# Kernel optimization log

Measured on AMD Instinct MI355X. Metric: run time of the kernel, lower is better.

The kernel has to match this reference:

```python
import jax, jax.numpy as jnp
import numpy as np

EMBED_DIM = 1024
NUM_HEADS = 16
HEAD_DIM = EMBED_DIM // NUM_HEADS
B, S = 4, 2048


def setup_inputs() -> dict:
    key = jax.random.key(0)
    ks = jax.random.split(key, 11)
    sc = 1.0 / np.sqrt(EMBED_DIM)
    return {
        "query": jax.random.normal(ks[0], (B, S, EMBED_DIM), jnp.float32),
        "key": jax.random.normal(ks[1], (B, S, EMBED_DIM), jnp.float32),
        "value": jax.random.normal(ks[2], (B, S, EMBED_DIM), jnp.float32),
        "Wq": jax.random.normal(ks[3], (EMBED_DIM, EMBED_DIM), jnp.float32) * sc,
        "Wk": jax.random.normal(ks[4], (EMBED_DIM, EMBED_DIM), jnp.float32) * sc,
        "Wv": jax.random.normal(ks[5], (EMBED_DIM, EMBED_DIM), jnp.float32) * sc,
        "Wo": jax.random.normal(ks[6], (EMBED_DIM, EMBED_DIM), jnp.float32) * sc,
        "bq": jax.random.normal(ks[7], (EMBED_DIM,), jnp.float32) * 0.01,
        "bk": jax.random.normal(ks[8], (EMBED_DIM,), jnp.float32) * 0.01,
        "bv": jax.random.normal(ks[9], (EMBED_DIM,), jnp.float32) * 0.01,
        "bo": jax.random.normal(ks[10], (EMBED_DIM,), jnp.float32) * 0.01,
    }


def reference(query, key, value, Wq, Wk, Wv, Wo, bq, bk, bv, bo):
    # QKV projections: [B,S,E] @ [E,E] (torch Linear uses x @ W.T; here W stored pre-transposed)
    def split_heads(x):  # [B,S,E] -> [B,H,S,D]
        Bx, Sx, _ = x.shape
        return x.reshape(Bx, Sx, NUM_HEADS, HEAD_DIM).transpose(0, 2, 1, 3)

    Q = split_heads(query @ Wq + bq)
    K = split_heads(key @ Wk + bk)
    V = split_heads(value @ Wv + bv)

    scale = 1.0 / np.sqrt(HEAD_DIM).astype(np.float32)
    scores = jnp.einsum("bhqd,bhkd->bhqk", Q, K) * scale  # [B,H,Sq,Sk]
    attn = jax.nn.softmax(scores, axis=-1)
    ctx = jnp.einsum("bhqk,bhkd->bhqd", attn, V)  # [B,H,Sq,D]
    ctx = ctx.transpose(0, 2, 1, 3).reshape(query.shape[0], query.shape[1], EMBED_DIM)
    return ctx @ Wo + bo
```

## Files before the change

kernel.cpp:

```cpp
#include <hip/hip_runtime.h>
#include <hip/hip_bf16.h>

typedef unsigned short u16;
typedef unsigned int u32;
typedef __attribute__((ext_vector_type(8))) short bf16x8;
typedef __attribute__((ext_vector_type(4))) float f32x4;
typedef __attribute__((ext_vector_type(2))) unsigned u32x2v;

constexpr int Bn = 4;
constexpr int Sn = 2048;
constexpr int En = 1024;
constexpr int Hn = 16;
constexpr int Dn = 64;
constexpr int Kd = 1024;

__device__ __forceinline__ u16 f2b(float f) {
  union { float f; unsigned u; } v; v.f = f;
  unsigned u = v.u;
  return (u16)((u + 0x7fffu + ((u >> 16) & 1u)) >> 16);
}

__device__ __forceinline__ u32 cvtpk_bf16(float lo, float hi) {
  u32 r;
  asm("v_cvt_pk_bf16_f32 %0, %1, %2" : "=v"(r) : "v"(lo), "v"(hi));
  return r;
}

__device__ __forceinline__ void gl_lds16(const u16* g, u16* l) {
  __builtin_amdgcn_global_load_lds(
      (const __attribute__((address_space(1))) void*)g,
      (__attribute__((address_space(3))) void*)l, 16, 0, 0);
}

__device__ __forceinline__ void plchain(u32& a, u32& b) {
  u32x2v s = __builtin_amdgcn_permlane32_swap(a, b, false, false);
  u32x2v t = __builtin_amdgcn_permlane16_swap(s[0], s[1], false, false);
  a = t[0]; b = t[1];
}

__device__ __forceinline__ float redsum_cross(float r) {
  union { float f; u32 u; } v; v.f = r;
  u32x2v s = __builtin_amdgcn_permlane32_swap(v.u, v.u, false, false);
  union { u32 u; float f; } x, y;
  x.u = s[0]; y.u = s[1];
  float m = x.f + y.f;
  union { float f; u32 u; } w; w.f = m;
  u32x2v t = __builtin_amdgcn_permlane16_swap(w.u, w.u, false, false);
  x.u = t[0]; y.u = t[1];
  return x.f + y.f;
}

__global__ __launch_bounds__(256) void conv_act(const float* __restrict__ in,
                                                u16* __restrict__ out, int n8) {
  int i = blockIdx.x * blockDim.x + threadIdx.x;
  const int stride = gridDim.x * blockDim.x;
  for (; i < n8; i += stride) {
    const float4* p = (const float4*)(in + (size_t)i * 8);
    float4 a = p[0], b = p[1];
    union { u32 w[4]; bf16x8 v; } r;
    r.w[0] = cvtpk_bf16(a.x, a.y); r.w[1] = cvtpk_bf16(a.z, a.w);
    r.w[2] = cvtpk_bf16(b.x, b.y); r.w[3] = cvtpk_bf16(b.z, b.w);
    *(bf16x8*)(out + (size_t)i * 8) = r.v;
  }
}

__global__ __launch_bounds__(256) void conv_wt3(
    const float* __restrict__ W0, const float* __restrict__ W1,
    const float* __restrict__ W2, u16* __restrict__ T0,
    u16* __restrict__ T1, u16* __restrict__ T2) {
  const float* W = (blockIdx.z == 0) ? W0 : (blockIdx.z == 1) ? W1 : W2;
  u16* Wt = (blockIdx.z == 0) ? T0 : (blockIdx.z == 1) ? T1 : T2;
  __shared__ float ts[64][65];
  const int t = threadIdx.x;
  const int k0 = blockIdx.y * 64, n0 = blockIdx.x * 64;
  const int r = t >> 4, c4 = (t & 15) * 4;
  #pragma unroll
  for (int i = 0; i < 4; i++) {
    float4 v = *(const float4*)&W[(size_t)(k0 + i * 16 + r) * En + n0 + c4];
    ts[i * 16 + r][c4 + 0] = v.x;
    ts[i * 16 + r][c4 + 1] = v.y;
    ts[i * 16 + r][c4 + 2] = v.z;
    ts[i * 16 + r][c4 + 3] = v.w;
  }
  __syncthreads();
  const int n = t >> 2, kc = (t & 3) * 16;
  u32 w8[8];
  #pragma unroll
  for (int j = 0; j < 8; j++)
    w8[j] = cvtpk_bf16(ts[kc + 2 * j][n], ts[kc + 2 * j + 1][n]);
  *(bf16x8*)&Wt[(size_t)(n0 + n) * Kd + k0 + kc]     = *(bf16x8*)&w8[0];
  *(bf16x8*)&Wt[(size_t)(n0 + n) * Kd + k0 + kc + 8] = *(bf16x8*)&w8[4];
}

__global__ __launch_bounds__(256) void conv_wt(const float* __restrict__ W,
                                               u16* __restrict__ Wt) {
  __shared__ float ts[64][65];
  const int t = threadIdx.x;
  const int k0 = blockIdx.y * 64, n0 = blockIdx.x * 64;
  const int r = t >> 4, c4 = (t & 15) * 4;
  #pragma unroll
  for (int i = 0; i < 4; i++) {
    float4 v = *(const float4*)&W[(size_t)(k0 + i * 16 + r) * En + n0 + c4];
    ts[i * 16 + r][c4 + 0] = v.x;
    ts[i * 16 + r][c4 + 1] = v.y;
    ts[i * 16 + r][c4 + 2] = v.z;
    ts[i * 16 + r][c4 + 3] = v.w;
  }
  __syncthreads();
  const int n = t >> 2, kc = (t & 3) * 16;
  u32 w8[8];
  #pragma unroll
  for (int j = 0; j < 8; j++)
    w8[j] = cvtpk_bf16(ts[kc + 2 * j][n], ts[kc + 2 * j + 1][n]);
  *(bf16x8*)&Wt[(size_t)(n0 + n) * Kd + k0 + kc]     = *(bf16x8*)&w8[0];
  *(bf16x8*)&Wt[(size_t)(n0 + n) * Kd + k0 + kc + 8] = *(bf16x8*)&w8[4];
}

template<int OUT_MODE>
__global__ __launch_bounds__(256) void gemm_k(
    const u16* __restrict__ A, const u16* __restrict__ Bt,
    const float* __restrict__ biasp, void* __restrict__ Cp, float alpha)
{
  constexpr int BK = 64;
  __shared__ u16 As[128 * BK];
  __shared__ u16 Bs[128 * BK];
  const int tid = threadIdx.x;
  const int lane = tid & 63, wave = tid >> 6;
  const int sid = (blockIdx.x & 7) * 64 + (blockIdx.x >> 3);
  const int brow = (sid >> 3) * 128, bcol = (sid & 7) * 128;
  const int wrow = (wave >> 1) * 64, wcol = (wave & 1) * 64;
  const int fr = lane & 15, fk = (lane >> 4) * 8, rq = (lane >> 4) * 4;

  const int lr = lane >> 3, lc = (lane & 7) * 8;
  const u16* Ag = A  + (size_t)(brow + 32 * wave + lr) * Kd + lc;
  const u16* Bg = Bt + (size_t)(bcol + 32 * wave + lr) * Kd + lc;
  u16* Asw = &As[(32 * wave) * BK];
  u16* Bsw = &Bs[(32 * wave) * BK];

  f32x4 acc[4][4] = {};

  for (int kt = 0; kt < Kd; kt += BK) {
    __syncthreads();
    #pragma unroll
    for (int i = 0; i < 4; i++) {
      gl_lds16(Ag + kt + (size_t)(8 * i) * Kd, Asw + (8 * i) * BK);
      gl_lds16(Bg + kt + (size_t)(8 * i) * Kd, Bsw + (8 * i) * BK);
    }
    __syncthreads();
    bf16x8 af[4][2], bfv[4][2];
    #pragma unroll
    for (int m = 0; m < 4; m++)
      #pragma unroll
      for (int ks = 0; ks < 2; ks++)
        af[m][ks] = *(const bf16x8*)&As[(wrow + m * 16 + fr) * BK + ks * 32 + fk];
    #pragma unroll
    for (int n = 0; n < 4; n++)
      #pragma unroll
      for (int ks = 0; ks < 2; ks++)
        bfv[n][ks] = *(const bf16x8*)&Bs[(wcol + n * 16 + fr) * BK + ks * 32 + fk];
    #pragma unroll
    for (int ks = 0; ks < 2; ks++)
      #pragma unroll
      for (int m = 0; m < 4; m++)
        #pragma unroll
        for (int n = 0; n < 4; n++)
          acc[m][n] = __builtin_amdgcn_mfma_f32_16x16x32_bf16(af[m][ks], bfv[n][ks], acc[m][n], 0, 0, 0);
  }

  #pragma unroll
  for (int m = 0; m < 4; m++) {
    #pragma unroll
    for (int n = 0; n < 4; n++) {
      const int row0 = brow + wrow + m * 16 + rq;
      const int col  = bcol + wcol + n * 16 + fr;
      const float bi = biasp[col];
      if constexpr (OUT_MODE == 0) {
        #pragma unroll
        for (int j = 0; j < 4; j++)
          ((float*)Cp)[(size_t)(row0 + j) * En + col] = (acc[m][n][j] + bi) * alpha;
      } else if constexpr (OUT_MODE == 1) {
        #pragma unroll
        for (int j = 0; j < 4; j++)
          ((u16*)Cp)[(size_t)(row0 + j) * En + col] = f2b((acc[m][n][j] + bi) * alpha);
      } else {
        u16 t4[4];
        #pragma unroll
        for (int j = 0; j < 4; j++) t4[j] = f2b((acc[m][n][j] + bi) * alpha);
        int bb = row0 >> 11, s = row0 & (Sn - 1);
        int hh = col >> 6, d = col & (Dn - 1);
        uint2 pk;
        pk.x = (u32)t4[0] | ((u32)t4[1] << 16);
        pk.y = (u32)t4[2] | ((u32)t4[3] << 16);
        *(uint2*)&((u16*)Cp)[((size_t)(bb * Hn + hh) * Dn + d) * Sn + s] = pk;
      }
    }
  }
}

#define SWZ(row, unit) (((row) * 64) + ((((unit) ^ ((row) & 7))) * 8))

__global__ __launch_bounds__(256) void attn_k(
    const u16* __restrict__ Qw, const u16* __restrict__ Kw,
    const u16* __restrict__ Vt, u16* __restrict__ Cw)
{
  constexpr int KB = 64, NT = Sn / KB, TSZ = 64 * 64;
  __shared__ u16 Ks[2 * TSZ];
  __shared__ u16 Vs[2 * TSZ];
  const int tid = threadIdx.x, lane = tid & 63, wave = tid >> 6;
  const int id = blockIdx.x;
  const int w = id >> 3;
  const int bh = (id & 7) * 8 + (w >> 3);
  const int qb = w & 7;
  const int b = bh >> 4, h = bh & 15;
  const int qbase = qb * 256 + wave * 64;
  const int fr = lane & 15, fk = (lane >> 4) * 8, rq = (lane >> 4) * 4;
  const int g = lane >> 4;

  const u16* Qg  = Qw + (size_t)(b * Sn + qbase) * En + h * Dn;
  const u16* Kg0 = Kw + (size_t)(b * Sn) * En + h * Dn;
  const u16* Vg0 = Vt + (size_t)bh * Dn * Sn;

  bf16x8 qf[4][2];
  #pragma unroll
  for (int qm = 0; qm < 4; qm++)
    #pragma unroll
    for (int ds = 0; ds < 2; ds++)
      qf[qm][ds] = *(const bf16x8*)&Qg[(size_t)(qm * 16 + fr) * En + ds * 32 + fk];

  float li_s[4] = {0.f, 0.f, 0.f, 0.f};
  f32x4 o[4][4] = {};

  const int sr0 = 16 * wave + (lane >> 3);
  const int su  = (lane & 7);

  auto stage = [&](int kv, int bufi) {
    #pragma unroll
    for (int c = 0; c < 2; c++) {
      const int r = sr0 + 8 * c;
      const int u = su ^ (r & 7);
      gl_lds16(Kg0 + (size_t)(kv + r) * En + u * 8, &Ks[bufi * TSZ + (16 * wave + 8 * c) * 64]);
      gl_lds16(Vg0 + (size_t)r * Sn + kv + u * 8,   &Vs[bufi * TSZ + (16 * wave + 8 * c) * 64]);
    }
  };

  stage(0, 0);
  int cur = 0;

  for (int t = 0; t < NT; t++) {
    asm volatile("s_waitcnt vmcnt(0)" ::: "memory");
    __syncthreads();
    if (t + 1 < NT) stage((t + 1) * KB, cur ^ 1);

    f32x4 st[4][4] = {};
    const u16* kbase = &Ks[cur * TSZ];
    #pragma unroll
    for (int kb = 0; kb < 4; kb++)
      #pragma unroll
      for (int ds = 0; ds < 2; ds++) {
        bf16x8 kf = *(const bf16x8*)&kbase[SWZ(kb * 16 + fr, ds * 4 + g)];
        #pragma unroll
        for (int qm = 0; qm < 4; qm++)
          st[kb][qm] = __builtin_amdgcn_mfma_f32_16x16x32_bf16(kf, qf[qm][ds], st[kb][qm], 0, 0, 0);
      }

    bf16x8 pa[4][2];
    #pragma unroll
    for (int qm = 0; qm < 4; qm++) {
      float p[4][4];
      #pragma unroll
      for (int kb = 0; kb < 4; kb++)
        #pragma unroll
        for (int j = 0; j < 4; j++)
          p[kb][j] = __builtin_amdgcn_exp2f(st[kb][qm][j]);
      float s0 = (p[0][0] + p[0][1]) + (p[0][2] + p[0][3]);
      float s1 = (p[1][0] + p[1][1]) + (p[1][2] + p[1][3]);
      float s2 = (p[2][0] + p[2][1]) + (p[2][2] + p[2][3]);
      float s3 = (p[3][0] + p[3][1]) + (p[3][2] + p[3][3]);
      li_s[qm] += redsum_cross((s0 + s1) + (s2 + s3));

      u32 plo[4], phi[4];
      #pragma unroll
      for (int kb = 0; kb < 4; kb++) {
        plo[kb] = cvtpk_bf16(p[kb][0], p[kb][1]);
        phi[kb] = cvtpk_bf16(p[kb][2], p[kb][3]);
      }
      plchain(plo[0], plo[1]);
      plchain(phi[0], phi[1]);
      plchain(plo[2], plo[3]);
      plchain(phi[2], phi[3]);
      union { u32 w[4]; bf16x8 v; } A0, A1;
      A0.w[0] = plo[0]; A0.w[1] = phi[0]; A0.w[2] = plo[1]; A0.w[3] = phi[1];
      A1.w[0] = plo[2]; A1.w[1] = phi[2]; A1.w[2] = plo[3]; A1.w[3] = phi[3];
      pa[qm][0] = A0.v;
      pa[qm][1] = A1.v;
    }

    {
      const u16* vbase = &Vs[cur * TSZ];
      #pragma unroll
      for (int nd = 0; nd < 4; nd++)
        #pragma unroll
        for (int ks = 0; ks < 2; ks++) {
          bf16x8 vf = *(const bf16x8*)&vbase[SWZ(nd * 16 + fr, ks * 4 + g)];
          #pragma unroll
          for (int qm = 0; qm < 4; qm++)
            o[qm][nd] = __builtin_amdgcn_mfma_f32_16x16x32_bf16(pa[qm][ks], vf, o[qm][nd], 0, 0, 0);
        }
    }
    cur ^= 1;
  }

  #pragma unroll
  for (int qm = 0; qm < 4; qm++) {
    float inv = 1.0f / li_s[qm];
    float rinv[4];
    #pragma unroll
    for (int j = 0; j < 4; j++) rinv[j] = __shfl(inv, (lane & 0x30) | (rq + j));
    #pragma unroll
    for (int nd = 0; nd < 4; nd++)
      #pragma unroll
      for (int j = 0; j < 4; j++) {
        int s = qbase + qm * 16 + rq + j;
        int d = nd * 16 + fr;
        Cw[((size_t)(b * Sn + s)) * En + h * Dn + d] = f2b(o[qm][nd][j] * rinv[j]);
      }
  }
}

extern "C" void kernel_launch(void* const* d_in, const int* in_sizes, int n_in,
                              void* d_out, int out_size, void* d_ws, size_t ws_size,
                              hipStream_t stream) {
  const float* q  = (const float*)d_in[0];
  const float* k  = (const float*)d_in[1];
  const float* v  = (const float*)d_in[2];
  const float* Wq = (const float*)d_in[3];
  const float* Wk = (const float*)d_in[4];
  const float* Wv = (const float*)d_in[5];
  const float* Wo = (const float*)d_in[6];
  const float* bq = (const float*)d_in[7];
  const float* bk = (const float*)d_in[8];
  const float* bv = (const float*)d_in[9];
  const float* bo = (const float*)d_in[10];

  const size_t NE = (size_t)Bn * Sn * En;
  const size_t WE = (size_t)En * En;
  u16* Qbf = (u16*)d_ws;
  u16* Kbf = Qbf + NE;
  u16* Vtw = Kbf + NE;
  u16* Cws = Vtw + NE;
  u16* Xact = (u16*)d_out;
  u16* WtQ  = Xact + NE;
  u16* WtK  = WtQ + WE;
  u16* WtV  = WtK + WE;
  u16* WtO  = Qbf;

  dim3 blk(256);
  dim3 gwt3(16, 16, 3);
  const int n8 = (int)(NE / 8);
  const float aq = 0.125f * 1.44269504088896340736f;

  conv_wt3<<<gwt3, blk, 0, stream>>>(Wq, Wk, Wv, WtQ, WtK, WtV);

  conv_act<<<2048, blk, 0, stream>>>(q, Xact, n8);
  gemm_k<1><<<512, blk, 0, stream>>>(Xact, WtQ, bq, Qbf, aq);

  conv_act<<<2048, blk, 0, stream>>>(k, Xact, n8);
  gemm_k<1><<<512, blk, 0, stream>>>(Xact, WtK, bk, Kbf, 1.0f);

  conv_act<<<2048, blk, 0, stream>>>(v, Xact, n8);
  gemm_k<2><<<512, blk, 0, stream>>>(Xact, WtV, bv, Vtw, 1.0f);

  attn_k<<<dim3(8 * Bn * Hn), blk, 0, stream>>>(Qbf, Kbf, Vtw, Cws);

  conv_wt<<<dim3(16, 16), blk, 0, stream>>>(Wo, WtO);
  gemm_k<0><<<512, blk, 0, stream>>>(Cws, WtO, bo, d_out, 1.0f);
}
```

Before: 237.3 us.

## Stagger KV start per block, batch LDS fragment loads, raise MFMA priority

Half the blocks now start their KV sweep at the midpoint of the sequence, spreading concurrent reads over different K/V regions. All K and V fragments for a tile are loaded from LDS into registers before the MFMA loops, so LDS latency is exposed once per tile rather than interleaved with each MFMA group. The MFMA sections are wrapped in s_setprio so those waves get issue priority. The cost is more live registers, which can lower occupancy. The softmax has no max subtraction, so the order of KV tiles does not change the result.

```diff
diff --git a/kernel.cpp b/kernel.cpp
--- a/kernel.cpp
+++ b/kernel.cpp
@@ -215,6 +215,7 @@
   const int qbase = qb * 256 + wave * 64;
   const int fr = lane & 15, fk = (lane >> 4) * 8, rq = (lane >> 4) * 4;
   const int g = lane >> 4;
+  const int st0 = ((id >> 3) & 1) * (NT / 2);
 
   const u16* Qg  = Qw + (size_t)(b * Sn + qbase) * En + h * Dn;
   const u16* Kg0 = Kw + (size_t)(b * Sn) * En + h * Dn;
@@ -243,25 +244,34 @@
     }
   };
 
-  stage(0, 0);
+  stage(st0 * KB, 0);
   int cur = 0;
 
   for (int t = 0; t < NT; t++) {
+    const int tt  = (t + st0) & (NT - 1);
+    const int ttn = (t + 1 + st0) & (NT - 1);
     asm volatile("s_waitcnt vmcnt(0)" ::: "memory");
     __syncthreads();
-    if (t + 1 < NT) stage((t + 1) * KB, cur ^ 1);
+    if (t + 1 < NT) stage(ttn * KB, cur ^ 1);
+    (void)tt;
 
     f32x4 st[4][4] = {};
     const u16* kbase = &Ks[cur * TSZ];
+    bf16x8 kf[4][2];
     #pragma unroll
     for (int kb = 0; kb < 4; kb++)
       #pragma unroll
-      for (int ds = 0; ds < 2; ds++) {
-        bf16x8 kf = *(const bf16x8*)&kbase[SWZ(kb * 16 + fr, ds * 4 + g)];
+      for (int ds = 0; ds < 2; ds++)
+        kf[kb][ds] = *(const bf16x8*)&kbase[SWZ(kb * 16 + fr, ds * 4 + g)];
+    __builtin_amdgcn_s_setprio(1);
+    #pragma unroll
+    for (int kb = 0; kb < 4; kb++)
+      #pragma unroll
+      for (int ds = 0; ds < 2; ds++)
         #pragma unroll
         for (int qm = 0; qm < 4; qm++)
-          st[kb][qm] = __builtin_amdgcn_mfma_f32_16x16x32_bf16(kf, qf[qm][ds], st[kb][qm], 0, 0, 0);
-      }
+          st[kb][qm] = __builtin_amdgcn_mfma_f32_16x16x32_bf16(kf[kb][ds], qf[qm][ds], st[kb][qm], 0, 0, 0);
+    __builtin_amdgcn_s_setprio(0);
 
     bf16x8 pa[4][2];
     #pragma unroll
@@ -297,15 +307,21 @@
 
     {
       const u16* vbase = &Vs[cur * TSZ];
+      bf16x8 vf[4][2];
       #pragma unroll
       for (int nd = 0; nd < 4; nd++)
         #pragma unroll
-        for (int ks = 0; ks < 2; ks++) {
-          bf16x8 vf = *(const bf16x8*)&vbase[SWZ(nd * 16 + fr, ks * 4 + g)];
+        for (int ks = 0; ks < 2; ks++)
+          vf[nd][ks] = *(const bf16x8*)&vbase[SWZ(nd * 16 + fr, ks * 4 + g)];
+      __builtin_amdgcn_s_setprio(1);
+      #pragma unroll
+      for (int nd = 0; nd < 4; nd++)
+        #pragma unroll
+        for (int ks = 0; ks < 2; ks++)
           #pragma unroll
           for (int qm = 0; qm < 4; qm++)
-            o[qm][nd] = __builtin_amdgcn_mfma_f32_16x16x32_bf16(pa[qm][ks], vf, o[qm][nd], 0, 0, 0);
-        }
+            o[qm][nd] = __builtin_amdgcn_mfma_f32_16x16x32_bf16(pa[qm][ks], vf[nd][ks], o[qm][nd], 0, 0, 0);
+      __builtin_amdgcn_s_setprio(0);
     }
     cur ^= 1;
   }
```

Result: slower. 259.6 us (+9.4%).

## Fuse fp32-to-bf16 activation conversion into QKV projection GEMM loads

Applied to the files above, without the earlier changes.

Removes the three standalone conv_act kernels and has the QKV GEMMs read fp32 activations directly. Each GEMM converts them to bf16 in registers and stores them into LDS, prefetching the next K tile into registers during the current compute. This drops a full write and re-read of a bf16 activation copy plus three launches. In exchange the A tile is loaded by plain vector loads instead of direct-to-LDS loads, and the kernel reads twice the bytes per A element and uses more registers for the prefetch.

```diff
diff --git a/kernel.cpp b/kernel.cpp
--- a/kernel.cpp
+++ b/kernel.cpp
@@ -50,20 +50,6 @@
   return x.f + y.f;
 }
 
-__global__ __launch_bounds__(256) void conv_act(const float* __restrict__ in,
-                                                u16* __restrict__ out, int n8) {
-  int i = blockIdx.x * blockDim.x + threadIdx.x;
-  const int stride = gridDim.x * blockDim.x;
-  for (; i < n8; i += stride) {
-    const float4* p = (const float4*)(in + (size_t)i * 8);
-    float4 a = p[0], b = p[1];
-    union { u32 w[4]; bf16x8 v; } r;
-    r.w[0] = cvtpk_bf16(a.x, a.y); r.w[1] = cvtpk_bf16(a.z, a.w);
-    r.w[2] = cvtpk_bf16(b.x, b.y); r.w[3] = cvtpk_bf16(b.z, b.w);
-    *(bf16x8*)(out + (size_t)i * 8) = r.v;
-  }
-}
-
 __global__ __launch_bounds__(256) void conv_wt3(
     const float* __restrict__ W0, const float* __restrict__ W1,
     const float* __restrict__ W2, u16* __restrict__ T0,
@@ -116,9 +102,9 @@
   *(bf16x8*)&Wt[(size_t)(n0 + n) * Kd + k0 + kc + 8] = *(bf16x8*)&w8[4];
 }
 
-template<int OUT_MODE>
+template<int OUT_MODE, bool A_F32>
 __global__ __launch_bounds__(256) void gemm_k(
-    const u16* __restrict__ A, const u16* __restrict__ Bt,
+    const void* __restrict__ Ap, const u16* __restrict__ Bt,
     const float* __restrict__ biasp, void* __restrict__ Cp, float alpha)
 {
   constexpr int BK = 64;
@@ -132,19 +118,48 @@
   const int fr = lane & 15, fk = (lane >> 4) * 8, rq = (lane >> 4) * 4;
 
   const int lr = lane >> 3, lc = (lane & 7) * 8;
-  const u16* Ag = A  + (size_t)(brow + 32 * wave + lr) * Kd + lc;
+  const u16* Ag = (const u16*)Ap + (size_t)(brow + 32 * wave + lr) * Kd + lc;
   const u16* Bg = Bt + (size_t)(bcol + 32 * wave + lr) * Kd + lc;
   u16* Asw = &As[(32 * wave) * BK];
   u16* Bsw = &Bs[(32 * wave) * BK];
 
+  const int arow = tid >> 1, ak0 = (tid & 1) * 32;
+  const float* Ag32 = (const float*)Ap + (size_t)(brow + arow) * Kd + ak0;
+
+  float4 x[8];
+  if constexpr (A_F32) {
+    #pragma unroll
+    for (int i = 0; i < 8; i++) x[i] = *(const float4*)(Ag32 + i * 4);
+  }
+
   f32x4 acc[4][4] = {};
 
   for (int kt = 0; kt < Kd; kt += BK) {
     __syncthreads();
-    #pragma unroll
-    for (int i = 0; i < 4; i++) {
-      gl_lds16(Ag + kt + (size_t)(8 * i) * Kd, Asw + (8 * i) * BK);
-      gl_lds16(Bg + kt + (size_t)(8 * i) * Kd, Bsw + (8 * i) * BK);
+    if constexpr (A_F32) {
+      #pragma unroll
+      for (int i = 0; i < 4; i++)
+        gl_lds16(Bg + kt + (size_t)(8 * i) * Kd, Bsw + (8 * i) * BK);
+      u32 w[16];
+      #pragma unroll
+      for (int i = 0; i < 8; i++) {
+        w[2 * i]     = cvtpk_bf16(x[i].x, x[i].y);
+        w[2 * i + 1] = cvtpk_bf16(x[i].z, x[i].w);
+      }
+      u16* dst = &As[arow * BK + ak0];
+      #pragma unroll
+      for (int j = 0; j < 4; j++)
+        *(bf16x8*)(dst + j * 8) = *(bf16x8*)&w[4 * j];
+      if (kt + BK < Kd) {
+        #pragma unroll
+        for (int i = 0; i < 8; i++) x[i] = *(const float4*)(Ag32 + kt + BK + i * 4);
+      }
+    } else {
+      #pragma unroll
+      for (int i = 0; i < 4; i++) {
+        gl_lds16(Ag + kt + (size_t)(8 * i) * Kd, Asw + (8 * i) * BK);
+        gl_lds16(Bg + kt + (size_t)(8 * i) * Kd, Bsw + (8 * i) * BK);
+      }
     }
     __syncthreads();
     bf16x8 af[4][2], bfv[4][2];
@@ -348,30 +363,23 @@
   u16* Kbf = Qbf + NE;
   u16* Vtw = Kbf + NE;
   u16* Cws = Vtw + NE;
-  u16* Xact = (u16*)d_out;
-  u16* WtQ  = Xact + NE;
+  u16* WtQ  = (u16*)d_out;
   u16* WtK  = WtQ + WE;
   u16* WtV  = WtK + WE;
   u16* WtO  = Qbf;
 
   dim3 blk(256);
   dim3 gwt3(16, 16, 3);
-  const int n8 = (int)(NE / 8);
   const float aq = 0.125f * 1.44269504088896340736f;
 
   conv_wt3<<<gwt3, blk, 0, stream>>>(Wq, Wk, Wv, WtQ, WtK, WtV);
 
-  conv_act<<<2048, blk, 0, stream>>>(q, Xact, n8);
-  gemm_k<1><<<512, blk, 0, stream>>>(Xact, WtQ, bq, Qbf, aq);
-
-  conv_act<<<2048, blk, 0, stream>>>(k, Xact, n8);
-  gemm_k<1><<<512, blk, 0, stream>>>(Xact, WtK, bk, Kbf, 1.0f);
-
-  conv_act<<<2048, blk, 0, stream>>>(v, Xact, n8);
-  gemm_k<2><<<512, blk, 0, stream>>>(Xact, WtV, bv, Vtw, 1.0f);
+  gemm_k<1, true><<<512, blk, 0, stream>>>(q, WtQ, bq, Qbf, aq);
+  gemm_k<1, true><<<512, blk, 0, stream>>>(k, WtK, bk, Kbf, 1.0f);
+  gemm_k<2, true><<<512, blk, 0, stream>>>(v, WtV, bv, Vtw, 1.0f);
 
   attn_k<<<dim3(8 * Bn * Hn), blk, 0, stream>>>(Qbf, Kbf, Vtw, Cws);
 
   conv_wt<<<dim3(16, 16), blk, 0, stream>>>(Wo, WtO);
-  gemm_k<0><<<512, blk, 0, stream>>>(Cws, WtO, bo, d_out, 1.0f);
-}
+  gemm_k<0, false><<<512, blk, 0, stream>>>(Cws, WtO, bo, d_out, 1.0f);
+}
```

Measured after the change: 258.5 us. +8.9%, slower.
